# Optimization experiments

Hardware: AMD Instinct MI355X
Metric: run time of the kernel (lower is better)

## Reference

```python
import jax, jax.numpy as jnp
import numpy as np

D_MODEL = 1024
N_HEADS = 16
BLOCK = 256
NEG = -1e9


def setup_inputs() -> dict:
    key = jax.random.key(0)
    ks = jax.random.split(key, 5)
    B, S, D = 4, 4096, D_MODEL
    scale = 0.02
    inp = {
        "x": jax.random.normal(ks[0], (B, S, D), dtype=jnp.float32),
        "Wq": jax.random.normal(ks[1], (D, D), dtype=jnp.float32) * scale,
        "bq": jnp.zeros((D,), dtype=jnp.float32),
        "Wk": jax.random.normal(ks[2], (D, D), dtype=jnp.float32) * scale,
        "bk": jnp.zeros((D,), dtype=jnp.float32),
        "Wv": jax.random.normal(ks[3], (D, D), dtype=jnp.float32) * scale,
        "bv": jnp.zeros((D,), dtype=jnp.float32),
        "Wo": jax.random.normal(ks[4], (D, D), dtype=jnp.float32) * scale,
        "bo": jnp.zeros((D,), dtype=jnp.float32),
    }
    return inp


def _local_attention(x, Wq, bq, Wk, bk, Wv, bv, Wo, bo):
    B, S, D = x.shape
    h, dh, bs = N_HEADS, D // N_HEADS, BLOCK
    pad_len = (bs - S % bs) % bs
    if pad_len > 0:
        x = jnp.pad(x, ((0, 0), (0, pad_len), (0, 0)))
    Sp = x.shape[1]
    nb = Sp // bs
    # independent local blocks: [B*nb, bs, D]
    xb = x.reshape(B * nb, bs, D)

    def proj(W, b):
        # [N, bs, D] -> [N, h, bs, dh]
        y = xb @ W + b
        return y.reshape(B * nb, bs, h, dh).transpose(0, 2, 1, 3)

    q = proj(Wq, bq)
    k = proj(Wk, bk)
    v = proj(Wv, bv)

    scores = jnp.einsum('nhqd,nhkd->nhqk', q, k) / jnp.sqrt(jnp.asarray(dh, x.dtype))
    causal = jnp.tril(jnp.ones((bs, bs), dtype=bool))  # block-local causal mask
    scores = jnp.where(causal, scores, jnp.asarray(NEG, x.dtype))
    probs = jax.nn.softmax(scores, axis=-1)
    out = jnp.einsum('nhqk,nhkd->nhqd', probs, v)
    out = out.transpose(0, 2, 1, 3).reshape(B, Sp, D)
    if pad_len > 0:
        out = out[:, :S, :]
    return out @ Wo + bo


def reference(x, Wq, bq, Wk, bk, Wv, bv, Wo, bo):
    return _local_attention(x, Wq, bq, Wk, bk, Wv, bv, Wo, bo)
```

## Files before the change

kernel.cpp:

```cpp
#include <hip/hip_runtime.h>
#include <cstdint>
#include <cstddef>

typedef unsigned short u16;
typedef __attribute__((ext_vector_type(8))) short s16x8;
typedef __attribute__((ext_vector_type(8))) unsigned short u16x8;
typedef __attribute__((ext_vector_type(4))) float f32x4;

#define D_MODEL 1024
#define DH 64
#define BS 256

__device__ __forceinline__ u16 f2bf(float f) {
  union { float f; unsigned int i; } x; x.f = f;
  unsigned int r = x.i + 0x7fffu + ((x.i >> 16) & 1u);
  return (u16)(r >> 16);
}

__device__ __forceinline__ void gl_lds16(const u16* g, u16* l) {
  __builtin_amdgcn_global_load_lds((const __attribute__((address_space(1))) void*)g,
                                   (__attribute__((address_space(3))) void*)l, 16, 0, 0);
}

__device__ __forceinline__ unsigned lds_off(const u16* p) {
  return (unsigned)(uintptr_t)(const __attribute__((address_space(3))) u16*)p;
}

__global__ __launch_bounds__(256) void cast_x(const float* __restrict__ x, u16* __restrict__ xb) {
  int i = (blockIdx.x * 256 + threadIdx.x) * 8;
  f32x4 a0 = *(const f32x4*)(x + i);
  f32x4 a1 = *(const f32x4*)(x + i + 4);
  u16x8 v;
#pragma unroll
  for (int j = 0; j < 4; ++j) { v[j] = f2bf(a0[j]); v[j + 4] = f2bf(a1[j]); }
  *(u16x8*)(xb + i) = v;
}

__global__ __launch_bounds__(256) void transpose_w(const float* __restrict__ w0,
                                                   const float* __restrict__ w1,
                                                   const float* __restrict__ w2,
                                                   const float* __restrict__ w3,
                                                   u16* __restrict__ out) {
  __shared__ u16 tile[64][65];
  const int z = blockIdx.z;
  const float* W = (z == 0) ? w0 : (z == 1) ? w1 : (z == 2) ? w2 : w3;
  u16* O = out + (size_t)z * (D_MODEL * D_MODEL);
  const int kb = blockIdx.y * 64, nb = blockIdx.x * 64;
  const int t = threadIdx.x;
#pragma unroll
  for (int i = 0; i < 16; ++i) {
    int e = i * 256 + t;
    int r = e >> 6, c = e & 63;
    tile[r][c] = f2bf(W[(size_t)(kb + r) * D_MODEL + nb + c]);
  }
  __syncthreads();
#pragma unroll
  for (int i = 0; i < 16; ++i) {
    int e = i * 256 + t;
    int r = e >> 6, c = e & 63;
    O[(size_t)(nb + r) * D_MODEL + kb + c] = tile[c][r];
  }
}


#define TIU 16384
#define HIU 8192

__device__ __forceinline__ void stage_half(const u16* __restrict__ src, int rowG0, int k0,
                                           u16* ldst, int tid) {
#pragma unroll
  for (int i = 0; i < 2; ++i) {
    int c = i * 512 + tid;
    int cs = c ^ ((c >> 3) & 7);
    gl_lds16(src + (size_t)(rowG0 + (cs >> 3)) * D_MODEL + k0 + (cs & 7) * 8,
             ldst + c * 8);
  }
}

#define NOPX ((void)0)
#define BARX() __builtin_amdgcn_s_barrier()
#define VMW(N) asm volatile("s_waitcnt vmcnt(" #N ")" ::: "memory")
#define SBAR() __builtin_amdgcn_sched_barrier(0)
#define LGK8() asm volatile("s_waitcnt lgkmcnt(8)")

#define DSR128(dst, b, off) asm volatile("ds_read_b128 %0, %1 offset:" #off : "=v"(dst) : "v"(b))

#define LDA8(P, MH) do { \
  const unsigned _o = (P) * 32768u + (MH) * 8192u; \
  DSR128(a[0][0], aK0 + _o, 0);    DSR128(a[0][1], aK1 + _o, 0); \
  DSR128(a[1][0], aK0 + _o, 2048); DSR128(a[1][1], aK1 + _o, 2048); \
  DSR128(a[2][0], aK0 + _o, 4096); DSR128(a[2][1], aK1 + _o, 4096); \
  DSR128(a[3][0], aK0 + _o, 6144); DSR128(a[3][1], aK1 + _o, 6144); \
} while (0)

#define LDB4(P, NH) do { \
  const unsigned _o = (P) * 32768u + (NH) * 4096u; \
  DSR128(b[NH][0][0], bK0 + _o, 0);    DSR128(b[NH][0][1], bK1 + _o, 0); \
  DSR128(b[NH][1][0], bK0 + _o, 2048); DSR128(b[NH][1][1], bK1 + _o, 2048); \
} while (0)

#define MF16(MH, NH) do { \
  __builtin_amdgcn_s_setprio(1); \
  _Pragma("unroll") for (int kk = 0; kk < 2; ++kk) \
  _Pragma("unroll") for (int mt = 0; mt < 4; ++mt) \
  _Pragma("unroll") for (int nt = 0; nt < 2; ++nt) \
    acc[(MH) * 4 + mt][(NH) * 2 + nt] = __builtin_amdgcn_mfma_f32_16x16x32_bf16( \
        a[mt][kk], b[NH][nt][kk], acc[(MH) * 4 + mt][(NH) * 2 + nt], 0, 0, 0); \
  __builtin_amdgcn_s_setprio(0); \
} while (0)

#define STA(T, H) stage_half(A, rowBase + (H) * 128, (T) * 64, As + ((T) & 1) * TIU + (H) * HIU, t)
#define STB(T, H) stage_half(W, colBase + (H) * 128, (T) * 64, Bs + ((T) & 1) * TIU + (H) * HIU, t)

#define PWAIT() do { BARX(); asm volatile("s_waitcnt lgkmcnt(0)"); SBAR(); } while (0)

#define KTILE(P, S1, S2, S3, S4, WAIT) do { \
  LDA8(P, 0); LDB4(P, 0); S1; LGK8(); PWAIT();  MF16(0, 0); BARX(); \
  LDB4(P, 1);             S2; PWAIT();          MF16(0, 1); BARX(); \
  LDA8(P, 1);             S3; PWAIT();          MF16(1, 1); BARX(); \
                    S4; WAIT; BARX(); SBAR();   MF16(1, 0); BARX(); \
} while (0)

template <int MODE, int NCB>
__global__ __launch_bounds__(512, 2) void gemm8(
    const u16* __restrict__ A, const u16* __restrict__ W,
    const float* __restrict__ b0, const float* __restrict__ b1, const float* __restrict__ b2,
    void* __restrict__ o0, void* __restrict__ o1, void* __restrict__ o2) {
  __shared__ u16 As[2 * TIU];
  __shared__ u16 Bs[2 * TIU];

  const int nwg = gridDim.x;
  const int wg = blockIdx.x;
  const int swz = (wg & 7) * (nwg >> 3) + (wg >> 3);
  const int rowBase = (swz / NCB) * 256;
  const int colBase = (swz % NCB) * 256;

  const int t = threadIdx.x;
  const int wave = t >> 6, lane = t & 63, l15 = lane & 15, q4 = lane >> 4;
  const int wm = wave >> 2, wn = wave & 3;
  const int arow = wm * 128 + l15;
  const int brow = wn * 64 + l15;

  const unsigned swzc = (unsigned)((q4 ^ (l15 & 7)) << 4);
  const unsigned aK0 = lds_off(As) + (unsigned)arow * 128u + swzc;
  const unsigned aK1 = aK0 ^ 64u;
  const unsigned bK0 = lds_off(Bs) + (unsigned)brow * 128u + swzc;
  const unsigned bK1 = bK0 ^ 64u;

  f32x4 acc[8][4];
#pragma unroll
  for (int i = 0; i < 8; ++i)
#pragma unroll
    for (int j = 0; j < 4; ++j) acc[i][j] = {0.f, 0.f, 0.f, 0.f};

  s16x8 a[4][2];
  s16x8 b[2][2][2];

  STB(0, 0); STB(0, 1); STA(0, 0); STA(0, 1);
  VMW(4);
  STB(1, 0); STB(1, 1); STA(1, 0);
  VMW(6);
  BARX();

#pragma unroll 1
  for (int tg = 0; tg < 14; tg += 2) {
    KTILE(0, STA(tg + 1, 1), STB(tg + 2, 0), STB(tg + 2, 1), STA(tg + 2, 0), VMW(6));
    KTILE(1, STA(tg + 2, 1), STB(tg + 3, 0), STB(tg + 3, 1), STA(tg + 3, 0), VMW(6));
  }
  KTILE(0, STA(15, 1), NOPX, NOPX, NOPX, VMW(0));
  KTILE(1, NOPX, NOPX, NOPX, NOPX, NOPX);

  if constexpr (MODE == 0) {
    const int z = colBase >> 10;
    const float* bias = (z == 0) ? b0 : (z == 1) ? b1 : b2;
    u16* Out = (u16*)((z == 0) ? o0 : (z == 1) ? o1 : o2);
    const int colL = (colBase & 1023) + wn * 64;
    float bv[4];
#pragma unroll
    for (int ni = 0; ni < 4; ++ni) bv[ni] = bias[colL + ni * 16 + l15];
#pragma unroll
    for (int mi = 0; mi < 8; ++mi) {
#pragma unroll
      for (int r = 0; r < 4; ++r) {
        size_t row = (size_t)(rowBase + wm * 128 + mi * 16 + q4 * 4 + r);
#pragma unroll
        for (int ni = 0; ni < 4; ++ni)
          Out[row * D_MODEL + colL + ni * 16 + l15] = f2bf(acc[mi][ni][r] + bv[ni]);
      }
    }
  } else {
    float* Out = (float*)o0;
    const int colL = colBase + wn * 64;
    float bv[4];
#pragma unroll
    for (int ni = 0; ni < 4; ++ni) bv[ni] = b0[colL + ni * 16 + l15];
#pragma unroll
    for (int mi = 0; mi < 8; ++mi) {
#pragma unroll
      for (int r = 0; r < 4; ++r) {
        size_t row = (size_t)(rowBase + wm * 128 + mi * 16 + q4 * 4 + r);
#pragma unroll
        for (int ni = 0; ni < 4; ++ni)
          Out[row * D_MODEL + colL + ni * 16 + l15] = acc[mi][ni][r] + bv[ni];
      }
    }
  }
}

__global__ __launch_bounds__(128) void attn(const u16* __restrict__ Q, const u16* __restrict__ K,
                                            const u16* __restrict__ V, u16* __restrict__ O) {
  __shared__ u16 vt[64 * 264];
  __shared__ u16 pl[2 * 16 * 264];
  const int g = blockIdx.x;
  const int n = g >> 4, h = g & 15;
  const size_t base = (size_t)n * BS * D_MODEL + (size_t)h * DH;
  const u16* Qb = Q + base;
  const u16* Kb = K + base;
  const u16* Vb = V + base;
  u16* Ob = O + base;
  const int t = threadIdx.x, wave = t >> 6, lane = t & 63, l15 = lane & 15, q4 = lane >> 4;

#pragma unroll
  for (int i = 0; i < 16; ++i) {
    int p = i * 128 + t;
    int d = p & 63, tok8 = p >> 6;
    u16x8 v;
#pragma unroll
    for (int j = 0; j < 8; ++j) v[j] = Vb[(size_t)(tok8 * 8 + j) * D_MODEL + d];
    *(u16x8*)(vt + d * 264 + tok8 * 8) = v;
  }
  __syncthreads();

  u16* pw = pl + wave * 16 * 264;

  for (int pass = 0; pass < 8; ++pass) {
    const int r0 = pass * 32 + wave * 16;
    const int a = r0 >> 4;

    s16x8 aq[2];
#pragma unroll
    for (int kk = 0; kk < 2; ++kk)
      aq[kk] = *(const s16x8*)(Qb + (size_t)(r0 + l15) * D_MODEL + kk * 32 + q4 * 8);

    f32x4 sc[16];
#pragma unroll
    for (int i = 0; i < 16; ++i) sc[i] = {0.f, 0.f, 0.f, 0.f};

    __builtin_amdgcn_s_setprio(1);
#pragma unroll
    for (int nt = 0; nt < 16; ++nt) {
      if (nt <= a) {
#pragma unroll
        for (int kk = 0; kk < 2; ++kk) {
          s16x8 bk = *(const s16x8*)(Kb + (size_t)(nt * 16 + l15) * D_MODEL + kk * 32 + q4 * 8);
          sc[nt] = __builtin_amdgcn_mfma_f32_16x16x32_bf16(aq[kk], bk, sc[nt], 0, 0, 0);
        }
      }
    }
    __builtin_amdgcn_s_setprio(0);

    float mrow[4] = {-3e38f, -3e38f, -3e38f, -3e38f};
#pragma unroll
    for (int nt = 0; nt < 16; ++nt) {
      if (nt <= a) {
#pragma unroll
        for (int r = 0; r < 4; ++r) {
          int col = nt * 16 + l15;
          int row = r0 + q4 * 4 + r;
          float s = (col > row) ? -1.0e9f : sc[nt][r] * 0.125f;
          sc[nt][r] = s;
          mrow[r] = fmaxf(mrow[r], s);
        }
      }
    }
#pragma unroll
    for (int r = 0; r < 4; ++r)
#pragma unroll
      for (int off = 1; off < 16; off <<= 1)
        mrow[r] = fmaxf(mrow[r], __shfl_xor(mrow[r], off, 64));

    float lrow[4] = {0.f, 0.f, 0.f, 0.f};
#pragma unroll
    for (int nt = 0; nt < 16; ++nt) {
      if (nt <= a) {
#pragma unroll
        for (int r = 0; r < 4; ++r) {
          float e = exp2f((sc[nt][r] - mrow[r]) * 1.44269504f);
          sc[nt][r] = e;
          lrow[r] += e;
        }
      }
    }
#pragma unroll
    for (int r = 0; r < 4; ++r)
#pragma unroll
      for (int off = 1; off < 16; off <<= 1)
        lrow[r] += __shfl_xor(lrow[r], off, 64);

#pragma unroll
    for (int nt = 0; nt < 16; ++nt) {
      if (nt <= a) {
#pragma unroll
        for (int r = 0; r < 4; ++r)
          pw[(q4 * 4 + r) * 264 + nt * 16 + l15] = f2bf(sc[nt][r]);
      }
    }
    if ((a & 1) == 0) {
#pragma unroll
      for (int r = 0; r < 4; ++r)
        pw[(q4 * 4 + r) * 264 + (a + 1) * 16 + l15] = 0;
    }
    const int ktmax = (a + 2) >> 1;

    f32x4 oc[4];
#pragma unroll
    for (int i = 0; i < 4; ++i) oc[i] = {0.f, 0.f, 0.f, 0.f};
    __builtin_amdgcn_s_setprio(1);
#pragma unroll
    for (int kt = 0; kt < 8; ++kt) {
      if (kt < ktmax) {
        s16x8 ap = *(const s16x8*)(pw + l15 * 264 + kt * 32 + q4 * 8);
#pragma unroll
        for (int dt = 0; dt < 4; ++dt) {
          s16x8 bv = *(const s16x8*)(vt + (dt * 16 + l15) * 264 + kt * 32 + q4 * 8);
          oc[dt] = __builtin_amdgcn_mfma_f32_16x16x32_bf16(ap, bv, oc[dt], 0, 0, 0);
        }
      }
    }
    __builtin_amdgcn_s_setprio(0);

    float inv[4];
#pragma unroll
    for (int r = 0; r < 4; ++r) inv[r] = 1.0f / lrow[r];

#pragma unroll
    for (int dt = 0; dt < 4; ++dt)
#pragma unroll
      for (int r = 0; r < 4; ++r)
        pw[(q4 * 4 + r) * 264 + dt * 16 + l15] = f2bf(oc[dt][r] * inv[r]);
#pragma unroll
    for (int k = 0; k < 2; ++k) {
      int c2 = k * 64 + lane;
      int row = c2 >> 3, c8 = (c2 & 7) * 8;
      u16x8 v = *(const u16x8*)(pw + row * 264 + c8);
      *(u16x8*)(Ob + (size_t)(r0 + row) * D_MODEL + c8) = v;
    }
  }
}

extern "C" void kernel_launch(void* const* d_in, const int* in_sizes, int n_in,
                              void* d_out, int out_size, void* d_ws, size_t ws_size,
                              hipStream_t stream) {
  const float* x  = (const float*)d_in[0];
  const float* Wq = (const float*)d_in[1];
  const float* bq = (const float*)d_in[2];
  const float* Wk = (const float*)d_in[3];
  const float* bk = (const float*)d_in[4];
  const float* Wv = (const float*)d_in[5];
  const float* bv = (const float*)d_in[6];
  const float* Wo = (const float*)d_in[7];
  const float* bo = (const float*)d_in[8];
  float* out = (float*)d_out;

  u16* ws = (u16*)d_ws;
  u16* Wt = ws;
  u16* Xb = ws + (size_t)4 * 1048576;
  u16* Qw = Xb + (size_t)16777216;
  u16* Kw = Qw + (size_t)16777216;
  u16* Vw = Kw + (size_t)16777216;
  u16* Ow = Qw;

  cast_x<<<dim3(8192), 256, 0, stream>>>(x, Xb);
  transpose_w<<<dim3(16, 16, 4), 256, 0, stream>>>(Wq, Wk, Wv, Wo, Wt);
  gemm8<0, 12><<<dim3(768), 512, 0, stream>>>(Xb, Wt, bq, bk, bv, Qw, Kw, Vw);
  attn<<<dim3(64 * 16), 128, 0, stream>>>(Qw, Kw, Vw, Ow);
  gemm8<1, 4><<<dim3(256), 512, 0, stream>>>(Ow, Wt + (size_t)3 * 1048576, bo,
                                             nullptr, nullptr, out, nullptr, nullptr);
}
```

Measured before the change: 371.0 us.

## Write V pre-transposed from QKV GEMM and rebalance causal attention work

The QKV GEMM epilogue now writes V in a per-(block, head) transposed layout, [dh][tokens], so the attention kernel can read V^T straight from global memory. This drops the strided gather into LDS and the barrier that followed it. Attention is split into 2048 blocks of 256 threads. Each wave handles a pair of query tiles (a, 15-a) to balance the causal triangle's work across waves. The trade-off is that V^T operands now come from global/L2 instead of LDS, and the GEMM epilogue's V writes are narrower 4-element stores.

Measured after the change: 411.2 us. +10.8%, slower.

```diff
diff --git a/kernel.cpp b/kernel.cpp
--- a/kernel.cpp
+++ b/kernel.cpp
@@ -5,6 +5,7 @@
 typedef unsigned short u16;
 typedef __attribute__((ext_vector_type(8))) short s16x8;
 typedef __attribute__((ext_vector_type(8))) unsigned short u16x8;
+typedef __attribute__((ext_vector_type(4))) unsigned short u16x4;
 typedef __attribute__((ext_vector_type(4))) float f32x4;
 
 #define D_MODEL 1024
@@ -172,20 +173,40 @@
 
   if constexpr (MODE == 0) {
     const int z = colBase >> 10;
-    const float* bias = (z == 0) ? b0 : (z == 1) ? b1 : b2;
-    u16* Out = (u16*)((z == 0) ? o0 : (z == 1) ? o1 : o2);
     const int colL = (colBase & 1023) + wn * 64;
-    float bv[4];
-#pragma unroll
-    for (int ni = 0; ni < 4; ++ni) bv[ni] = bias[colL + ni * 16 + l15];
-#pragma unroll
-    for (int mi = 0; mi < 8; ++mi) {
-#pragma unroll
-      for (int r = 0; r < 4; ++r) {
-        size_t row = (size_t)(rowBase + wm * 128 + mi * 16 + q4 * 4 + r);
-#pragma unroll
-        for (int ni = 0; ni < 4; ++ni)
-          Out[row * D_MODEL + colL + ni * 16 + l15] = f2bf(acc[mi][ni][r] + bv[ni]);
+    if (z < 2) {
+      const float* bias = (z == 0) ? b0 : b1;
+      u16* Out = (u16*)((z == 0) ? o0 : o1);
+      float bv[4];
+#pragma unroll
+      for (int ni = 0; ni < 4; ++ni) bv[ni] = bias[colL + ni * 16 + l15];
+#pragma unroll
+      for (int mi = 0; mi < 8; ++mi) {
+#pragma unroll
+        for (int r = 0; r < 4; ++r) {
+          size_t row = (size_t)(rowBase + wm * 128 + mi * 16 + q4 * 4 + r);
+#pragma unroll
+          for (int ni = 0; ni < 4; ++ni)
+            Out[row * D_MODEL + colL + ni * 16 + l15] = f2bf(acc[mi][ni][r] + bv[ni]);
+        }
+      }
+    } else {
+      u16* Vt = (u16*)o2;
+      const int nIdx = rowBase >> 8;
+      float bv[4];
+#pragma unroll
+      for (int ni = 0; ni < 4; ++ni) bv[ni] = b2[colL + ni * 16 + l15];
+#pragma unroll
+      for (int mi = 0; mi < 8; ++mi) {
+        const int tk = wm * 128 + mi * 16 + q4 * 4;
+#pragma unroll
+        for (int ni = 0; ni < 4; ++ni) {
+          const int col = colL + ni * 16 + l15;
+          u16x4 v4;
+#pragma unroll
+          for (int r = 0; r < 4; ++r) v4[r] = f2bf(acc[mi][ni][r] + bv[ni]);
+          *(u16x4*)(Vt + (((size_t)nIdx * 16 + (col >> 6)) * 64 + (col & 63)) * 256 + tk) = v4;
+        }
       }
     }
   } else {
@@ -207,35 +228,25 @@
   }
 }
 
-__global__ __launch_bounds__(128) void attn(const u16* __restrict__ Q, const u16* __restrict__ K,
-                                            const u16* __restrict__ V, u16* __restrict__ O) {
-  __shared__ u16 vt[64 * 264];
-  __shared__ u16 pl[2 * 16 * 264];
+__global__ __launch_bounds__(256, 3) void attn(const u16* __restrict__ Q, const u16* __restrict__ K,
+                                               const u16* __restrict__ Vt, u16* __restrict__ O) {
+  __shared__ u16 pl[4 * 16 * 264];
   const int g = blockIdx.x;
-  const int n = g >> 4, h = g & 15;
+  const int nh = g >> 1, j = g & 1;
+  const int n = nh >> 4, h = nh & 15;
   const size_t base = (size_t)n * BS * D_MODEL + (size_t)h * DH;
   const u16* Qb = Q + base;
   const u16* Kb = K + base;
-  const u16* Vb = V + base;
+  const u16* Vb = Vt + (size_t)nh * (64 * 256);
   u16* Ob = O + base;
   const int t = threadIdx.x, wave = t >> 6, lane = t & 63, l15 = lane & 15, q4 = lane >> 4;
-
-#pragma unroll
-  for (int i = 0; i < 16; ++i) {
-    int p = i * 128 + t;
-    int d = p & 63, tok8 = p >> 6;
-    u16x8 v;
-#pragma unroll
-    for (int j = 0; j < 8; ++j) v[j] = Vb[(size_t)(tok8 * 8 + j) * D_MODEL + d];
-    *(u16x8*)(vt + d * 264 + tok8 * 8) = v;
-  }
-  __syncthreads();
-
+  const int slot = j * 4 + wave;
   u16* pw = pl + wave * 16 * 264;
 
-  for (int pass = 0; pass < 8; ++pass) {
-    const int r0 = pass * 32 + wave * 16;
-    const int a = r0 >> 4;
+#pragma unroll 1
+  for (int pi = 0; pi < 2; ++pi) {
+    const int a = pi ? (15 - slot) : slot;
+    const int r0 = a * 16;
 
     s16x8 aq[2];
 #pragma unroll
@@ -322,7 +333,7 @@
         s16x8 ap = *(const s16x8*)(pw + l15 * 264 + kt * 32 + q4 * 8);
 #pragma unroll
         for (int dt = 0; dt < 4; ++dt) {
-          s16x8 bv = *(const s16x8*)(vt + (dt * 16 + l15) * 264 + kt * 32 + q4 * 8);
+          s16x8 bv = *(const s16x8*)(Vb + (size_t)(dt * 16 + l15) * 256 + kt * 32 + q4 * 8);
           oc[dt] = __builtin_amdgcn_mfma_f32_16x16x32_bf16(ap, bv, oc[dt], 0, 0, 0);
         }
       }
@@ -373,7 +384,7 @@
   cast_x<<<dim3(8192), 256, 0, stream>>>(x, Xb);
   transpose_w<<<dim3(16, 16, 4), 256, 0, stream>>>(Wq, Wk, Wv, Wo, Wt);
   gemm8<0, 12><<<dim3(768), 512, 0, stream>>>(Xb, Wt, bq, bk, bv, Qw, Kw, Vw);
-  attn<<<dim3(64 * 16), 128, 0, stream>>>(Qw, Kw, Vw, Ow);
+  attn<<<dim3(2048), 256, 0, stream>>>(Qw, Kw, Vw, Ow);
   gemm8<1, 4><<<dim3(256), 512, 0, stream>>>(Ow, Wt + (size_t)3 * 1048576, bo,
                                              nullptr, nullptr, out, nullptr, nullptr);
 }
```
